# Optimization experiments

Hardware: AMD Instinct MI355X
Metric: run time of the kernel (lower is better)

Reference implementation:

```python
import jax, jax.numpy as jnp
import numpy as np
import itertools

N_FEATURES = 256
BATCH = 4096
SAME_DIVIDER = 1

def _pair_indices(n_features, same_divider):
    pairs = [(i, j) for i, j in itertools.combinations(range(n_features), 2)
             if i // same_divider != j // same_divider]
    a = np.array([p[0] for p in pairs], dtype=np.int32)
    b = np.array([p[1] for p in pairs], dtype=np.int32)
    return a, b

def setup_inputs() -> dict:
    key = jax.random.key(0)
    x = jax.random.normal(key, (BATCH, N_FEATURES), dtype=jnp.float32)
    a, b = _pair_indices(N_FEATURES, SAME_DIVIDER)  # [32640] each
    return {"x": x, "idx_a": jnp.asarray(a), "idx_b": jnp.asarray(b)}

def reference(x, idx_a, idx_b):
    # pairwise_fn='mul': crossed features are x[:, i] * x[:, j] for each pair (i, j)
    crossed = x[:, idx_a] * x[:, idx_b]          # [B, n_pairs]
    return jnp.concatenate([x, crossed], axis=1)  # [B, F + n_pairs]
```

## Files before the change

kernel.cpp:

```cpp
#include <hip/hip_runtime.h>

#define NF     256
#define NPAIRS 32640
#define OUTW   (NF + NPAIRS)
#define BATCH  4096

__global__ __launch_bounds__(256)
void poly_features_kernel(const float* __restrict__ x,
                          const int*   __restrict__ idx_a,
                          const int*   __restrict__ idx_b,
                          float*       __restrict__ out)
{
    __shared__ float sx[NF];

    const int b = blockIdx.x;
    const int t = threadIdx.x;

    const float* xrow = x + (size_t)b * NF;
    float v = xrow[t];
    sx[t] = v;

    float* orow = out + (size_t)b * OUTW;
    orow[t] = v;

    __syncthreads();

    const int4* ia4 = (const int4*)idx_a;
    const int4* ib4 = (const int4*)idx_b;
    float4* o4 = (float4*)(orow + NF);

    #pragma unroll 4
    for (int g = t; g < NPAIRS / 4; g += 256) {
        int4 ia = ia4[g];
        int4 ib = ib4[g];
        float4 r;
        r.x = sx[ia.x] * sx[ib.x];
        r.y = sx[ia.y] * sx[ib.y];
        r.z = sx[ia.z] * sx[ib.z];
        r.w = sx[ia.w] * sx[ib.w];
        o4[g] = r;
    }
}

extern "C" void kernel_launch(void* const* d_in, const int* in_sizes, int n_in,
                              void* d_out, int out_size, void* d_ws, size_t ws_size,
                              hipStream_t stream) {
    const float* x     = (const float*)d_in[0];
    const int*   idx_a = (const int*)d_in[1];
    const int*   idx_b = (const int*)d_in[2];
    float*       out   = (float*)d_out;

    poly_features_kernel<<<BATCH, 256, 0, stream>>>(x, idx_a, idx_b, out);
}
```

Before: 549.8 us.

## Compute pair products from triangular structure instead of gathering index arrays

Drops the per-element reads of idx_a/idx_b and instead generates the upper-triangular pair layout directly. For each row feature i, threads t>i write x[i]*x[t] to a contiguous segment of the output at a computed offset. This removes large repeated index traffic through L2 and the shared-memory gathers. In exchange, stores become scalar and unaligned, and the triangular predicate idles about half the lanes. It also assumes the index arrays always follow itertools.combinations order.

Result: slower. 631.9 us (+14.9%).

```diff
diff --git a/kernel.cpp b/kernel.cpp
--- a/kernel.cpp
+++ b/kernel.cpp
@@ -16,29 +16,29 @@
     const int b = blockIdx.x;
     const int t = threadIdx.x;
 
-    const float* xrow = x + (size_t)b * NF;
-    float v = xrow[t];
+    const float v = x[(size_t)b * NF + t];
     sx[t] = v;
 
-    float* orow = out + (size_t)b * OUTW;
+    float* __restrict__ orow = out + (size_t)b * OUTW;
     orow[t] = v;
 
     __syncthreads();
 
-    const int4* ia4 = (const int4*)idx_a;
-    const int4* ib4 = (const int4*)idx_b;
-    float4* o4 = (float4*)(orow + NF);
+    float* __restrict__ ox = orow + NF;
+    float* __restrict__ pt = ox + t;
 
-    #pragma unroll 4
-    for (int g = t; g < NPAIRS / 4; g += 256) {
-        int4 ia = ia4[g];
-        int4 ib = ib4[g];
-        float4 r;
-        r.x = sx[ia.x] * sx[ib.x];
-        r.y = sx[ia.y] * sx[ib.y];
-        r.z = sx[ia.z] * sx[ib.z];
-        r.w = sx[ia.w] * sx[ib.w];
-        o4[g] = r;
+    int off = 0;
+    for (int i0 = 0; i0 < 256; i0 += 4) {
+        const float4 s4 = *(const float4*)(&sx[i0]);
+        const float si[4] = {s4.x, s4.y, s4.z, s4.w};
+        #pragma unroll
+        for (int k = 0; k < 4; ++k) {
+            const int i = i0 + k;
+            if (t > i) {
+                pt[off - i - 1] = si[k] * v;
+            }
+            off += 255 - i;
+        }
     }
 }
 
```
